# Kernel tuning notes

Measured on AMD Instinct MI355X. Metric: run time of the kernel, lower is better.

The kernel has to match this reference:

```python
import jax, jax.numpy as jnp
import numpy as np

N_NODES = 50000
N_EDGES = 1_600_000
F_IN = 128
HIDDEN = 128
N_REL = 8
N_GRAPHS = 64


def setup_inputs() -> dict:
    key = jax.random.key(0)
    ks = jax.random.split(key, 16)
    x = jax.random.normal(ks[0], (N_NODES, F_IN), dtype=jnp.float32)
    edge_index = jax.random.randint(ks[1], (2, N_EDGES), 0, N_NODES, dtype=jnp.int32)
    edge_type = jax.random.randint(ks[2], (N_EDGES,), 0, N_REL, dtype=jnp.int32)
    edge_attr = jax.nn.one_hot(edge_type, N_REL, dtype=jnp.float32)  # one-hot relation encoding
    batch = jnp.sort(jax.random.randint(ks[3], (N_NODES,), 0, N_GRAPHS, dtype=jnp.int32))
    s = 1.0 / np.sqrt(F_IN)
    params = {}
    dims = [(F_IN, HIDDEN), (HIDDEN, HIDDEN), (HIDDEN, HIDDEN)]
    for i, (fi, fo) in enumerate(dims, 1):
        params[f"W{i}"] = jax.random.normal(ks[3 + 3 * i], (N_REL, fi, fo), dtype=jnp.float32) * s
        params[f"root{i}"] = jax.random.normal(ks[4 + 3 * i], (fi, fo), dtype=jnp.float32) * s
        params[f"b{i}"] = jnp.zeros((fo,), dtype=jnp.float32)
    lin_w = jax.random.normal(ks[13], (HIDDEN, HIDDEN), dtype=jnp.float32) * (1.0 / np.sqrt(HIDDEN))
    lin_b = jnp.zeros((HIDDEN,), dtype=jnp.float32)
    return {"x": x, "edge_index": edge_index, "edge_attr": edge_attr, "batch": batch,
            **params, "lin_w": lin_w, "lin_b": lin_b}


def _rgcn_conv(x, src, dst, edge_type, W, root, bias):
    # PyG RGCNConv with aggr='mean': per-relation mean of transformed neighbors + root + bias.
    # Mean is linear, so aggregate raw features per (dst, relation) then apply W_r.
    n = x.shape[0]
    seg = dst * N_REL + edge_type                      # combined segment id [E]
    msg = x[src]                                       # [E, F_in] gather
    agg = jax.ops.segment_sum(msg, seg, num_segments=n * N_REL)
    cnt = jax.ops.segment_sum(jnp.ones((src.shape[0],), x.dtype), seg, num_segments=n * N_REL)
    agg = agg / jnp.maximum(cnt, 1.0)[:, None]
    agg = agg.reshape(n, N_REL, -1)                    # [N, R, F_in]
    return jnp.einsum('nri,rio->no', agg, W) + x @ root + bias


def reference(x, edge_index, edge_attr, batch,
              W1, root1, b1, W2, root2, b2, W3, root3, b3, lin_w, lin_b):
    src, dst = edge_index[0], edge_index[1]
    edge_type = jnp.argmax(edge_attr, axis=1)          # np.where(edge_attr == 1)[1]
    h = jax.nn.relu(_rgcn_conv(x, src, dst, edge_type, W1, root1, b1))
    h = jax.nn.relu(_rgcn_conv(h, src, dst, edge_type, W2, root2, b2))
    h = jax.nn.relu(_rgcn_conv(h, src, dst, edge_type, W3, root3, b3))
    # global_mean_pool over graphs
    sums = jax.ops.segment_sum(h, batch, num_segments=N_GRAPHS)
    cnts = jax.ops.segment_sum(jnp.ones((h.shape[0],), h.dtype), batch, num_segments=N_GRAPHS)
    pooled = sums / jnp.maximum(cnts, 1.0)[:, None]    # [G, hidden]
    return pooled @ lin_w + lin_b
```

## Files before the change

### kernel.cpp

```cpp
#include <hip/hip_runtime.h>
#include <hip/hip_fp16.h>

#define N_NODESC 50000
#define N_EDGESC 1600000
#define FEAT 128
#define NREL 8
#define NSEG (N_NODESC * NREL)
#define NGRAPH 64
#define KTOT 1152
#define NKC 36
#define WPACK_ELEMS (NKC * 4 * 128 * 8)
#define NHALF (N_NODESC * FEAT)

typedef float f32x4 __attribute__((ext_vector_type(4)));
typedef _Float16 f16x8 __attribute__((ext_vector_type(8)));

static inline size_t align256(size_t x) { return (x + 255) & ~(size_t)255; }

__device__ __forceinline__ float4 h4tof4(uint2 r) {
  const __half* h = (const __half*)&r;
  return make_float4(__half2float(h[0]), __half2float(h[1]),
                     __half2float(h[2]), __half2float(h[3]));
}

__global__ void k_zero(int* __restrict__ p, int n) {
  int i = blockIdx.x * blockDim.x + threadIdx.x;
  int stride = gridDim.x * blockDim.x;
  for (; i < n; i += stride) p[i] = 0;
}

__global__ void k_cvt16(const float* __restrict__ in, __half* __restrict__ o) {
  int i = blockIdx.x * blockDim.x + threadIdx.x;
  if (i * 4 >= NHALF) return;
  float4 v = *(const float4*)&in[i * 4];
  __half h[4] = {__float2half(v.x), __float2half(v.y), __float2half(v.z), __float2half(v.w)};
  *(uint2*)&o[(size_t)i * 4] = *(uint2*)h;
}

__global__ void k_edge_hist(const int* __restrict__ ei, const float* __restrict__ eattr,
                            int* __restrict__ seg, int* __restrict__ cnt) {
  int e = blockIdx.x * blockDim.x + threadIdx.x;
  if (e >= N_EDGESC) return;
  int dst = ei[N_EDGESC + e];
  const float4* ap = (const float4*)(eattr + (size_t)e * 8);
  float4 a0 = ap[0], a1 = ap[1];
  int ty = 0;
  if (a0.y > 0.5f) ty = 1;
  if (a0.z > 0.5f) ty = 2;
  if (a0.w > 0.5f) ty = 3;
  if (a1.x > 0.5f) ty = 4;
  if (a1.y > 0.5f) ty = 5;
  if (a1.z > 0.5f) ty = 6;
  if (a1.w > 0.5f) ty = 7;
  int s = dst * NREL + ty;
  seg[e] = s;
  atomicAdd(&cnt[s], 1);
}

__global__ void k_scan1(const int* __restrict__ cnt, int* __restrict__ outIncl,
                        int* __restrict__ bsums, int n) {
  __shared__ int sd[256];
  int t = threadIdx.x;
  int base = blockIdx.x * 4096 + t * 16;
  int v[16];
  int s = 0;
#pragma unroll
  for (int j = 0; j < 16; ++j) {
    int idx = base + j;
    int x = (idx < n) ? cnt[idx] : 0;
    s += x;
    v[j] = s;
  }
  sd[t] = s;
  __syncthreads();
  for (int off = 1; off < 256; off <<= 1) {
    int add = (t >= off) ? sd[t - off] : 0;
    __syncthreads();
    sd[t] += add;
    __syncthreads();
  }
  int prev = (t > 0) ? sd[t - 1] : 0;
#pragma unroll
  for (int j = 0; j < 16; ++j) {
    int idx = base + j;
    if (idx < n) outIncl[idx] = prev + v[j];
  }
  if (t == 255) bsums[blockIdx.x] = sd[255];
}

__global__ void k_scan2(int* __restrict__ bsums, int nb) {
  __shared__ int sd[128];
  int t = threadIdx.x;
  int v = (t < nb) ? bsums[t] : 0;
  sd[t] = v;
  __syncthreads();
  for (int off = 1; off < 128; off <<= 1) {
    int add = (t >= off) ? sd[t - off] : 0;
    __syncthreads();
    sd[t] += add;
    __syncthreads();
  }
  if (t < nb) bsums[t] = sd[t] - v;
}

__global__ void k_scan3(int* __restrict__ offsets, const int* __restrict__ bsums, int n) {
  int i = blockIdx.x * blockDim.x + threadIdx.x;
  if (i == 0) offsets[0] = 0;
  if (i < n) offsets[i + 1] += bsums[i >> 12];
}

__global__ void k_scatter(const int* __restrict__ ei, const int* __restrict__ seg,
                          const int* __restrict__ offsets, int* __restrict__ cursor,
                          int* __restrict__ ssrc) {
  int e = blockIdx.x * blockDim.x + threadIdx.x;
  if (e >= N_EDGESC) return;
  int s = seg[e];
  int p = offsets[s] + atomicAdd(&cursor[s], 1);
  ssrc[p] = ei[e];
}

__global__ __launch_bounds__(256, 8) void k_agg(
    const __half* __restrict__ in, const int* __restrict__ offsets,
    const int* __restrict__ ssrc, __half* __restrict__ agg,
    int nodeBase, int nodeCount) {
  int t = blockIdx.x * blockDim.x + threadIdx.x;
  int un = t >> 5;
  int l = t & 31;
  if (un >= nodeCount) return;
  int node = nodeBase + un;
  for (int r = 0; r < NREL; ++r) {
    int sidx = node * NREL + r;
    int beg = offsets[sidx], end = offsets[sidx + 1];
    float4 s = make_float4(0.f, 0.f, 0.f, 0.f);
    for (int base = beg; base < end; base += 4) {
      int last = end - 1;
      int e1 = base + 1 <= last ? base + 1 : last;
      int e2 = base + 2 <= last ? base + 2 : last;
      int e3 = base + 3 <= last ? base + 3 : last;
      int i0 = ssrc[base], i1 = ssrc[e1], i2 = ssrc[e2], i3 = ssrc[e3];
      uint2 r0 = *(const uint2*)&in[(size_t)i0 * FEAT + l * 4];
      uint2 r1 = *(const uint2*)&in[(size_t)i1 * FEAT + l * 4];
      uint2 r2 = *(const uint2*)&in[(size_t)i2 * FEAT + l * 4];
      uint2 r3 = *(const uint2*)&in[(size_t)i3 * FEAT + l * 4];
      float4 v0 = h4tof4(r0), v1 = h4tof4(r1), v2 = h4tof4(r2), v3 = h4tof4(r3);
      s.x += v0.x; s.y += v0.y; s.z += v0.z; s.w += v0.w;
      if (base + 1 < end) { s.x += v1.x; s.y += v1.y; s.z += v1.z; s.w += v1.w; }
      if (base + 2 < end) { s.x += v2.x; s.y += v2.y; s.z += v2.z; s.w += v2.w; }
      if (base + 3 < end) { s.x += v3.x; s.y += v3.y; s.z += v3.z; s.w += v3.w; }
    }
    int c = end - beg;
    if (c > 1) {
      float inv = 1.0f / (float)c;
      s.x *= inv; s.y *= inv; s.z *= inv; s.w *= inv;
    }
    __half hv[4] = {__float2half(s.x), __float2half(s.y), __float2half(s.z), __float2half(s.w)};
    *(uint2*)&agg[((size_t)un * NREL + r) * FEAT + l * 4] = *(uint2*)hv;
  }
}

__global__ void k_wpack(const float* __restrict__ W, const float* __restrict__ root,
                        __half* __restrict__ whi, __half* __restrict__ wlo) {
  int idx = blockIdx.x * 256 + threadIdx.x;
  if (idx >= WPACK_ELEMS) return;
  int j = idx & 7;
  int n = (idx >> 3) & 127;
  int slot = idx >> 10;
  int k = slot * 8 + j;
  float v = (k < 1024) ? W[(size_t)k * 128 + n] : root[(size_t)(k - 1024) * 128 + n];
  __half hi = __float2half(v);
  float lof = v - __half2float(hi);
  whi[idx] = hi;
  wlo[idx] = __float2half(lof);
}

__global__ __launch_bounds__(256, 4) void k_gemm_mfma(
    const __half* __restrict__ aggc,
    const __half* __restrict__ xin,
    const __half* __restrict__ Whi, const __half* __restrict__ Wlo,
    const float* __restrict__ bias, __half* __restrict__ out16,
    int n0g, int rows) {
  __shared__ __half Ah[4 * 128 * 8] __attribute__((aligned(16)));
  __shared__ __half Bh[4 * 128 * 8] __attribute__((aligned(16)));
  __shared__ __half Bl[4 * 128 * 8] __attribute__((aligned(16)));

  const int t = threadIdx.x;
  const int lane = t & 63, wave = t >> 6;
  const int l15 = lane & 15, lg = lane >> 4;
  const int wrow0 = wave * 32;
  const int m0 = blockIdx.x * 128;
  const int srow = t >> 1, half = t & 1;

  f32x4 acc[2][8];
#pragma unroll
  for (int a = 0; a < 2; ++a)
#pragma unroll
    for (int b = 0; b < 8; ++b) acc[a][b] = (f32x4){0.f, 0.f, 0.f, 0.f};

  for (int kc = 0; kc < NKC; ++kc) {
    int rowc = srow;
    if (m0 + rowc >= rows) rowc = rows - 1 - m0;
    if (rowc < 0) rowc = 0;
    const __half* asrc = (kc < 32)
        ? (aggc + (size_t)(m0 + rowc) * 1024 + kc * 32 + half * 16)
        : (xin + (size_t)(n0g + m0 + rowc) * FEAT + (kc - 32) * 32 + half * 16);
    uint4 av0 = ((const uint4*)asrc)[0];
    uint4 av1 = ((const uint4*)asrc)[1];
    const uint4* bhs = (const uint4*)(Whi + (size_t)kc * 4096);
    const uint4* bls = (const uint4*)(Wlo + (size_t)kc * 4096);
    uint4 bh0 = bhs[t * 2], bh1 = bhs[t * 2 + 1];
    uint4 bl0 = bls[t * 2], bl1 = bls[t * 2 + 1];

    __syncthreads();

    {
      int g0 = half * 2;
      *(uint4*)&Ah[((size_t)(g0 * 128 + srow)) * 8] = av0;
      *(uint4*)&Ah[((size_t)((g0 + 1) * 128 + srow)) * 8] = av1;
      ((uint4*)Bh)[t * 2] = bh0;
      ((uint4*)Bh)[t * 2 + 1] = bh1;
      ((uint4*)Bl)[t * 2] = bl0;
      ((uint4*)Bl)[t * 2 + 1] = bl1;
    }
    __syncthreads();

    f16x8 af[2];
#pragma unroll
    for (int mf = 0; mf < 2; ++mf) {
      int ar = wrow0 + mf * 16 + l15;
      af[mf] = *(const f16x8*)&Ah[((size_t)(lg * 128 + ar)) * 8];
    }
#pragma unroll
    for (int nf = 0; nf < 8; ++nf) {
      int bn = nf * 16 + l15;
      f16x8 bh = *(const f16x8*)&Bh[((size_t)(lg * 128 + bn)) * 8];
      f16x8 bl = *(const f16x8*)&Bl[((size_t)(lg * 128 + bn)) * 8];
#pragma unroll
      for (int mf = 0; mf < 2; ++mf) {
        acc[mf][nf] = __builtin_amdgcn_mfma_f32_16x16x32_f16(af[mf], bh, acc[mf][nf], 0, 0, 0);
        acc[mf][nf] = __builtin_amdgcn_mfma_f32_16x16x32_f16(af[mf], bl, acc[mf][nf], 0, 0, 0);
      }
    }
  }

  float bcol[8];
#pragma unroll
  for (int nf = 0; nf < 8; ++nf) bcol[nf] = bias[nf * 16 + l15];
#pragma unroll
  for (int mf = 0; mf < 2; ++mf)
#pragma unroll
    for (int nf = 0; nf < 8; ++nf)
#pragma unroll
      for (int j = 0; j < 4; ++j) {
        int grow = m0 + wrow0 + mf * 16 + lg * 4 + j;
        if (grow < rows) {
          float v = acc[mf][nf][j] + bcol[nf];
          v = v > 0.f ? v : 0.f;
          out16[(size_t)(n0g + grow) * FEAT + nf * 16 + l15] = __float2half(v);
        }
      }
}

__global__ void k_pool(const __half* __restrict__ h, const int* __restrict__ batch,
                       const float* __restrict__ lw, const float* __restrict__ lb,
                       float* __restrict__ out) {
  __shared__ float sums[8][128];
  __shared__ float prow[128];
  int gidx = blockIdx.x, t = threadIdx.x;
  int f = t & 127, grp = t >> 7;
  int lo = 0, hi = N_NODESC;
  while (lo < hi) {
    int mid = (lo + hi) >> 1;
    if (batch[mid] < gidx) lo = mid + 1; else hi = mid;
  }
  int start = lo;
  hi = N_NODESC;
  while (lo < hi) {
    int mid = (lo + hi) >> 1;
    if (batch[mid] < gidx + 1) lo = mid + 1; else hi = mid;
  }
  int end = lo;
  float s = 0.f;
  for (int n = start + grp; n < end; n += 8) s += __half2float(h[(size_t)n * FEAT + f]);
  sums[grp][f] = s;
  __syncthreads();
  if (grp == 0) {
    float tot = 0.f;
#pragma unroll
    for (int gg = 0; gg < 8; ++gg) tot += sums[gg][f];
    int c = end - start;
    prow[f] = (c > 0) ? tot / (float)c : 0.f;
  }
  __syncthreads();
  float a = 0.f;
  for (int k = grp * 16; k < grp * 16 + 16; ++k) a = fmaf(prow[k], lw[(size_t)k * FEAT + f], a);
  __syncthreads();
  sums[grp][f] = a;
  __syncthreads();
  if (grp == 0) {
    float tot = lb[f];
#pragma unroll
    for (int gg = 0; gg < 8; ++gg) tot += sums[gg][f];
    out[(size_t)gidx * FEAT + f] = tot;
  }
}

extern "C" void kernel_launch(void* const* d_in, const int* in_sizes, int n_in,
                              void* d_out, int out_size, void* d_ws, size_t ws_size,
                              hipStream_t stream) {
  const float* x = (const float*)d_in[0];
  const int* ei = (const int*)d_in[1];
  const float* eattr = (const float*)d_in[2];
  const int* batch = (const int*)d_in[3];
  const float* Wl[3] = {(const float*)d_in[4], (const float*)d_in[7], (const float*)d_in[10]};
  const float* rl[3] = {(const float*)d_in[5], (const float*)d_in[8], (const float*)d_in[11]};
  const float* bl[3] = {(const float*)d_in[6], (const float*)d_in[9], (const float*)d_in[12]};
  const float* lw = (const float*)d_in[13];
  const float* lb = (const float*)d_in[14];
  float* out = (float*)d_out;
  (void)n_in; (void)in_sizes; (void)out_size;

  size_t pos = 0;
  char* base = (char*)d_ws;
  auto alloc = [&](size_t bytes) { char* q = base + pos; pos += align256(bytes); return q; };
  int* seg = (int*)alloc(sizeof(int) * (size_t)N_EDGESC);
  int* cntcur = (int*)alloc(sizeof(int) * (size_t)2 * NSEG);
  int* cnt = cntcur;
  int* cursor = cntcur + NSEG;
  int* offsets = (int*)alloc(sizeof(int) * (size_t)(NSEG + 1));
  int* bsums = (int*)alloc(sizeof(int) * 1024);
  int* ssrc = (int*)alloc(sizeof(int) * (size_t)N_EDGESC);
  __half* p0 = (__half*)alloc(sizeof(__half) * (size_t)NHALF);
  __half* p1 = (__half*)alloc(sizeof(__half) * (size_t)NHALF);
  __half* whi = (__half*)alloc(sizeof(__half) * (size_t)WPACK_ELEMS);
  __half* wlo = (__half*)alloc(sizeof(__half) * (size_t)WPACK_ELEMS);
  size_t remain = (ws_size > pos) ? (ws_size - pos) : 0;
  long long cn = (long long)(remain / (sizeof(__half) * NREL * FEAT));
  int chunkNodes = (cn > N_NODESC) ? N_NODESC : (int)cn;
  chunkNodes &= ~127;
  if (chunkNodes < 128) chunkNodes = 128;
  __half* aggbuf = (__half*)(base + pos);
  int nchunks = (N_NODESC + chunkNodes - 1) / chunkNodes;

  hipLaunchKernelGGL(k_zero, dim3(2048), dim3(256), 0, stream, cntcur, 2 * NSEG);
  hipLaunchKernelGGL(k_edge_hist, dim3((N_EDGESC + 255) / 256), dim3(256), 0, stream,
                     ei, eattr, seg, cnt);
  int nbScan = (NSEG + 4095) / 4096;
  hipLaunchKernelGGL(k_scan1, dim3(nbScan), dim3(256), 0, stream, cnt, offsets + 1, bsums, NSEG);
  hipLaunchKernelGGL(k_scan2, dim3(1), dim3(128), 0, stream, bsums, nbScan);
  hipLaunchKernelGGL(k_scan3, dim3((NSEG + 255) / 256), dim3(256), 0, stream, offsets, bsums, NSEG);
  hipLaunchKernelGGL(k_scatter, dim3((N_EDGESC + 255) / 256), dim3(256), 0, stream,
                     ei, seg, offsets, cursor, ssrc);

  hipLaunchKernelGGL(k_cvt16, dim3((NHALF / 4 + 255) / 256), dim3(256), 0, stream, x, p0);

  const __half* inPtr = p0;
  __half* outPtr = p1;
  for (int L = 0; L < 3; ++L) {
    hipLaunchKernelGGL(k_wpack, dim3((WPACK_ELEMS + 255) / 256), dim3(256), 0, stream,
                       Wl[L], rl[L], whi, wlo);
    for (int c = 0; c < nchunks; ++c) {
      int nodeBase = c * chunkNodes;
      int rowsC = N_NODESC - nodeBase;
      if (rowsC > chunkNodes) rowsC = chunkNodes;
      int aggBlocks = (rowsC * 32 + 255) / 256;
      hipLaunchKernelGGL(k_agg, dim3(aggBlocks), dim3(256), 0, stream,
                         inPtr, offsets, ssrc, aggbuf, nodeBase, rowsC);
      hipLaunchKernelGGL(k_gemm_mfma, dim3((rowsC + 127) / 128), dim3(256), 0, stream,
                         aggbuf, inPtr, whi, wlo, bl[L], outPtr, nodeBase, rowsC);
    }
    const __half* tmp = inPtr;
    inPtr = outPtr;
    outPtr = (__half*)tmp;
  }

  hipLaunchKernelGGL(k_pool, dim3(NGRAPH), dim3(1024), 0, stream, p1, batch, lw, lb, out);
}
```

Baseline: 790.0 us.

## Load MFMA operands directly from global memory, removing LDS staging and barriers

The GEMM kernel no longer stages A and B tiles through shared memory with two __syncthreads per K-chunk. Each lane now loads its f16x8 MFMA fragments straight from global memory, relying on the packed weight layout and L1/L2 caching. The K loop is split into an aggregate part and a root/x part so the per-iteration branch goes away. Launch bounds drop from 4 to 3 blocks per CU to give more registers. Each wave now loads the B fragments itself, so weight reads no longer come from a single per-block LDS copy, and global load latency is exposed without software pipelining.

After: 1.009 ms. 27.7% more time.

```diff
diff --git a/kernel.cpp b/kernel.cpp
--- a/kernel.cpp
+++ b/kernel.cpp
@@ -173,22 +173,29 @@
   wlo[idx] = __float2half(lof);
 }
 
-__global__ __launch_bounds__(256, 4) void k_gemm_mfma(
+__global__ __launch_bounds__(256, 3) void k_gemm_mfma(
     const __half* __restrict__ aggc,
     const __half* __restrict__ xin,
     const __half* __restrict__ Whi, const __half* __restrict__ Wlo,
     const float* __restrict__ bias, __half* __restrict__ out16,
     int n0g, int rows) {
-  __shared__ __half Ah[4 * 128 * 8] __attribute__((aligned(16)));
-  __shared__ __half Bh[4 * 128 * 8] __attribute__((aligned(16)));
-  __shared__ __half Bl[4 * 128 * 8] __attribute__((aligned(16)));
-
   const int t = threadIdx.x;
   const int lane = t & 63, wave = t >> 6;
   const int l15 = lane & 15, lg = lane >> 4;
   const int wrow0 = wave * 32;
   const int m0 = blockIdx.x * 128;
-  const int srow = t >> 1, half = t & 1;
+
+  int r0 = m0 + wrow0 + l15;
+  int r1 = r0 + 16;
+  if (r0 >= rows) r0 = rows - 1;
+  if (r1 >= rows) r1 = rows - 1;
+  const __half* a0p = aggc + (size_t)r0 * 1024 + lg * 8;
+  const __half* a1p = aggc + (size_t)r1 * 1024 + lg * 8;
+  const __half* x0p = xin + (size_t)(n0g + r0) * FEAT + lg * 8;
+  const __half* x1p = xin + (size_t)(n0g + r1) * FEAT + lg * 8;
+  const size_t bbase = (size_t)lg * 1024 + (size_t)l15 * 8;
+  const __half* bhp = Whi + bbase;
+  const __half* blp = Wlo + bbase;
 
   f32x4 acc[2][8];
 #pragma unroll
@@ -196,49 +203,34 @@
 #pragma unroll
     for (int b = 0; b < 8; ++b) acc[a][b] = (f32x4){0.f, 0.f, 0.f, 0.f};
 
-  for (int kc = 0; kc < NKC; ++kc) {
-    int rowc = srow;
-    if (m0 + rowc >= rows) rowc = rows - 1 - m0;
-    if (rowc < 0) rowc = 0;
-    const __half* asrc = (kc < 32)
-        ? (aggc + (size_t)(m0 + rowc) * 1024 + kc * 32 + half * 16)
-        : (xin + (size_t)(n0g + m0 + rowc) * FEAT + (kc - 32) * 32 + half * 16);
-    uint4 av0 = ((const uint4*)asrc)[0];
-    uint4 av1 = ((const uint4*)asrc)[1];
-    const uint4* bhs = (const uint4*)(Whi + (size_t)kc * 4096);
-    const uint4* bls = (const uint4*)(Wlo + (size_t)kc * 4096);
-    uint4 bh0 = bhs[t * 2], bh1 = bhs[t * 2 + 1];
-    uint4 bl0 = bls[t * 2], bl1 = bls[t * 2 + 1];
-
-    __syncthreads();
-
-    {
-      int g0 = half * 2;
-      *(uint4*)&Ah[((size_t)(g0 * 128 + srow)) * 8] = av0;
-      *(uint4*)&Ah[((size_t)((g0 + 1) * 128 + srow)) * 8] = av1;
-      ((uint4*)Bh)[t * 2] = bh0;
-      ((uint4*)Bh)[t * 2 + 1] = bh1;
-      ((uint4*)Bl)[t * 2] = bl0;
-      ((uint4*)Bl)[t * 2 + 1] = bl1;
-    }
-    __syncthreads();
-
-    f16x8 af[2];
-#pragma unroll
-    for (int mf = 0; mf < 2; ++mf) {
-      int ar = wrow0 + mf * 16 + l15;
-      af[mf] = *(const f16x8*)&Ah[((size_t)(lg * 128 + ar)) * 8];
-    }
+  for (int kc = 0; kc < 32; ++kc) {
+    f16x8 a0 = *(const f16x8*)(a0p + kc * 32);
+    f16x8 a1 = *(const f16x8*)(a1p + kc * 32);
+    const __half* bh = bhp + (size_t)kc * 4096;
+    const __half* bl = blp + (size_t)kc * 4096;
 #pragma unroll
     for (int nf = 0; nf < 8; ++nf) {
-      int bn = nf * 16 + l15;
-      f16x8 bh = *(const f16x8*)&Bh[((size_t)(lg * 128 + bn)) * 8];
-      f16x8 bl = *(const f16x8*)&Bl[((size_t)(lg * 128 + bn)) * 8];
-#pragma unroll
-      for (int mf = 0; mf < 2; ++mf) {
-        acc[mf][nf] = __builtin_amdgcn_mfma_f32_16x16x32_f16(af[mf], bh, acc[mf][nf], 0, 0, 0);
-        acc[mf][nf] = __builtin_amdgcn_mfma_f32_16x16x32_f16(af[mf], bl, acc[mf][nf], 0, 0, 0);
-      }
+      f16x8 vh = *(const f16x8*)(bh + nf * 128);
+      f16x8 vl = *(const f16x8*)(bl + nf * 128);
+      acc[0][nf] = __builtin_amdgcn_mfma_f32_16x16x32_f16(a0, vh, acc[0][nf], 0, 0, 0);
+      acc[0][nf] = __builtin_amdgcn_mfma_f32_16x16x32_f16(a0, vl, acc[0][nf], 0, 0, 0);
+      acc[1][nf] = __builtin_amdgcn_mfma_f32_16x16x32_f16(a1, vh, acc[1][nf], 0, 0, 0);
+      acc[1][nf] = __builtin_amdgcn_mfma_f32_16x16x32_f16(a1, vl, acc[1][nf], 0, 0, 0);
+    }
+  }
+  for (int kc = 0; kc < 4; ++kc) {
+    f16x8 a0 = *(const f16x8*)(x0p + kc * 32);
+    f16x8 a1 = *(const f16x8*)(x1p + kc * 32);
+    const __half* bh = bhp + (size_t)(kc + 32) * 4096;
+    const __half* bl = blp + (size_t)(kc + 32) * 4096;
+#pragma unroll
+    for (int nf = 0; nf < 8; ++nf) {
+      f16x8 vh = *(const f16x8*)(bh + nf * 128);
+      f16x8 vl = *(const f16x8*)(bl + nf * 128);
+      acc[0][nf] = __builtin_amdgcn_mfma_f32_16x16x32_f16(a0, vh, acc[0][nf], 0, 0, 0);
+      acc[0][nf] = __builtin_amdgcn_mfma_f32_16x16x32_f16(a0, vl, acc[0][nf], 0, 0, 0);
+      acc[1][nf] = __builtin_amdgcn_mfma_f32_16x16x32_f16(a1, vh, acc[1][nf], 0, 0, 0);
+      acc[1][nf] = __builtin_amdgcn_mfma_f32_16x16x32_f16(a1, vl, acc[1][nf], 0, 0, 0);
     }
   }
 
```

## Double-buffer LDS tiles and prefetch two K-chunks ahead in MFMA GEMM

Applied to the files above, without the earlier changes.

The GEMM kernel now keeps two LDS buffers for the A and B tiles. Global loads for chunk kc+2 are issued while MFMAs run on chunk kc, which leaves one barrier per iteration instead of two. The row clamp and base pointers are hoisted out of the loop. LDS usage doubles and the launch-bounds occupancy hint drops from 4 to 3 blocks per CU to make room for the extra state.

After: 744.6 us. 5.7% less time.

```diff
diff --git a/kernel.cpp b/kernel.cpp
--- a/kernel.cpp
+++ b/kernel.cpp
@@ -173,15 +173,15 @@
   wlo[idx] = __float2half(lof);
 }
 
-__global__ __launch_bounds__(256, 4) void k_gemm_mfma(
+__global__ __launch_bounds__(256, 3) void k_gemm_mfma(
     const __half* __restrict__ aggc,
     const __half* __restrict__ xin,
     const __half* __restrict__ Whi, const __half* __restrict__ Wlo,
     const float* __restrict__ bias, __half* __restrict__ out16,
     int n0g, int rows) {
-  __shared__ __half Ah[4 * 128 * 8] __attribute__((aligned(16)));
-  __shared__ __half Bh[4 * 128 * 8] __attribute__((aligned(16)));
-  __shared__ __half Bl[4 * 128 * 8] __attribute__((aligned(16)));
+  __shared__ __half Ah[2][4096] __attribute__((aligned(16)));
+  __shared__ __half Bh[2][4096] __attribute__((aligned(16)));
+  __shared__ __half Bl[2][4096] __attribute__((aligned(16)));
 
   const int t = threadIdx.x;
   const int lane = t & 63, wave = t >> 6;
@@ -190,57 +190,71 @@
   const int m0 = blockIdx.x * 128;
   const int srow = t >> 1, half = t & 1;
 
+  int rowc = srow;
+  if (m0 + rowc >= rows) rowc = rows - 1 - m0;
+  if (rowc < 0) rowc = 0;
+  const __half* aggRow = aggc + (size_t)(m0 + rowc) * 1024 + half * 16;
+  const __half* xRow = xin + (size_t)(n0g + m0 + rowc) * FEAT + half * 16;
+
+  uint4 av0, av1, sbh0, sbh1, sbl0, sbl1;
+
+#define LOADC(kc)                                                         \
+  {                                                                       \
+    const __half* asrc = ((kc) < 32) ? (aggRow + (kc) * 32)               \
+                                     : (xRow + ((kc) - 32) * 32);         \
+    av0 = ((const uint4*)asrc)[0];                                        \
+    av1 = ((const uint4*)asrc)[1];                                        \
+    const uint4* bhs = (const uint4*)(Whi + (size_t)(kc) * 4096);         \
+    const uint4* bls = (const uint4*)(Wlo + (size_t)(kc) * 4096);         \
+    sbh0 = bhs[t * 2]; sbh1 = bhs[t * 2 + 1];                             \
+    sbl0 = bls[t * 2]; sbl1 = bls[t * 2 + 1];                             \
+  }
+#define WRITEC(b)                                                         \
+  {                                                                       \
+    int g0 = half * 2;                                                    \
+    *(uint4*)&Ah[b][(g0 * 128 + srow) * 8] = av0;                         \
+    *(uint4*)&Ah[b][((g0 + 1) * 128 + srow) * 8] = av1;                   \
+    ((uint4*)Bh[b])[t * 2] = sbh0; ((uint4*)Bh[b])[t * 2 + 1] = sbh1;     \
+    ((uint4*)Bl[b])[t * 2] = sbl0; ((uint4*)Bl[b])[t * 2 + 1] = sbl1;     \
+  }
+
   f32x4 acc[2][8];
 #pragma unroll
   for (int a = 0; a < 2; ++a)
 #pragma unroll
     for (int b = 0; b < 8; ++b) acc[a][b] = (f32x4){0.f, 0.f, 0.f, 0.f};
 
+  LOADC(0);
+  WRITEC(0);
+  LOADC(1);
+  __syncthreads();
+
   for (int kc = 0; kc < NKC; ++kc) {
-    int rowc = srow;
-    if (m0 + rowc >= rows) rowc = rows - 1 - m0;
-    if (rowc < 0) rowc = 0;
-    const __half* asrc = (kc < 32)
-        ? (aggc + (size_t)(m0 + rowc) * 1024 + kc * 32 + half * 16)
-        : (xin + (size_t)(n0g + m0 + rowc) * FEAT + (kc - 32) * 32 + half * 16);
-    uint4 av0 = ((const uint4*)asrc)[0];
-    uint4 av1 = ((const uint4*)asrc)[1];
-    const uint4* bhs = (const uint4*)(Whi + (size_t)kc * 4096);
-    const uint4* bls = (const uint4*)(Wlo + (size_t)kc * 4096);
-    uint4 bh0 = bhs[t * 2], bh1 = bhs[t * 2 + 1];
-    uint4 bl0 = bls[t * 2], bl1 = bls[t * 2 + 1];
-
-    __syncthreads();
-
-    {
-      int g0 = half * 2;
-      *(uint4*)&Ah[((size_t)(g0 * 128 + srow)) * 8] = av0;
-      *(uint4*)&Ah[((size_t)((g0 + 1) * 128 + srow)) * 8] = av1;
-      ((uint4*)Bh)[t * 2] = bh0;
-      ((uint4*)Bh)[t * 2 + 1] = bh1;
-      ((uint4*)Bl)[t * 2] = bl0;
-      ((uint4*)Bl)[t * 2 + 1] = bl1;
-    }
-    __syncthreads();
-
+    const int cur = kc & 1;
     f16x8 af[2];
 #pragma unroll
     for (int mf = 0; mf < 2; ++mf) {
       int ar = wrow0 + mf * 16 + l15;
-      af[mf] = *(const f16x8*)&Ah[((size_t)(lg * 128 + ar)) * 8];
+      af[mf] = *(const f16x8*)&Ah[cur][(lg * 128 + ar) * 8];
     }
 #pragma unroll
     for (int nf = 0; nf < 8; ++nf) {
       int bn = nf * 16 + l15;
-      f16x8 bh = *(const f16x8*)&Bh[((size_t)(lg * 128 + bn)) * 8];
-      f16x8 bl = *(const f16x8*)&Bl[((size_t)(lg * 128 + bn)) * 8];
-#pragma unroll
-      for (int mf = 0; mf < 2; ++mf) {
-        acc[mf][nf] = __builtin_amdgcn_mfma_f32_16x16x32_f16(af[mf], bh, acc[mf][nf], 0, 0, 0);
-        acc[mf][nf] = __builtin_amdgcn_mfma_f32_16x16x32_f16(af[mf], bl, acc[mf][nf], 0, 0, 0);
-      }
-    }
-  }
+      f16x8 vh = *(const f16x8*)&Bh[cur][(lg * 128 + bn) * 8];
+      f16x8 vl = *(const f16x8*)&Bl[cur][(lg * 128 + bn) * 8];
+      acc[0][nf] = __builtin_amdgcn_mfma_f32_16x16x32_f16(af[0], vh, acc[0][nf], 0, 0, 0);
+      acc[0][nf] = __builtin_amdgcn_mfma_f32_16x16x32_f16(af[0], vl, acc[0][nf], 0, 0, 0);
+      acc[1][nf] = __builtin_amdgcn_mfma_f32_16x16x32_f16(af[1], vh, acc[1][nf], 0, 0, 0);
+      acc[1][nf] = __builtin_amdgcn_mfma_f32_16x16x32_f16(af[1], vl, acc[1][nf], 0, 0, 0);
+    }
+    if (kc < NKC - 1) {
+      WRITEC(cur ^ 1);
+      if (kc < NKC - 2) LOADC(kc + 2);
+      __syncthreads();
+    }
+  }
+#undef LOADC
+#undef WRITEC
 
   float bcol[8];
 #pragma unroll
```
